# Optimization experiments

Hardware: AMD Instinct MI355X
Metric: run time of the kernel (lower is better)

Reference implementation:

```python
import jax, jax.numpy as jnp
import numpy as np

EPS = 1e-5
DEPTH = 6
HEADS = 8
DIM_HEAD = 64

def layer_norm(x, g, b):
    m = jnp.mean(x, axis=-1, keepdims=True)
    v = jnp.mean((x - m) ** 2, axis=-1, keepdims=True)
    return (x - m) * jax.lax.rsqrt(v + EPS) * g + b

def setup_inputs() -> dict:
    key = jax.random.key(0)
    ks = jax.random.split(key, 12)
    b, T, F, v, D = 4, 8, 16, 196, 768
    L, inner, ffh = DEPTH, HEADS * DIM_HEAD, 4 * D
    s = 0.02
    return {
        "x": jax.random.normal(ks[0], (b, T, F, v, D), jnp.float32),
        "latents": jax.random.normal(ks[1], (64, D), jnp.float32),
        "frame_emb": jax.random.normal(ks[2], (F, D), jnp.float32),
        "time_emb": jax.random.normal(ks[3], (T, 1, D), jnp.float32),
        "ln_m_g": jnp.ones((L, D), jnp.float32),
        "ln_m_b": jnp.zeros((L, D), jnp.float32),
        "ln_l_g": jnp.ones((L, D), jnp.float32),
        "ln_l_b": jnp.zeros((L, D), jnp.float32),
        "Wq": jax.random.normal(ks[4], (L, D, inner), jnp.float32) * s,
        "Wk": jax.random.normal(ks[5], (L, D, inner), jnp.float32) * s,
        "Wv": jax.random.normal(ks[6], (L, D, inner), jnp.float32) * s,
        "Wo": jax.random.normal(ks[7], (L, inner, D), jnp.float32) * s,
        "ff_ln_g": jnp.ones((L, D), jnp.float32),
        "ff_ln_b": jnp.zeros((L, D), jnp.float32),
        "W1": jax.random.normal(ks[8], (L, D, ffh), jnp.float32) * s,
        "W2": jax.random.normal(ks[9], (L, ffh, D), jnp.float32) * s,
        "out_ln_g": jnp.ones((D,), jnp.float32),
        "out_ln_b": jnp.zeros((D,), jnp.float32),
    }

def perceiver_attention(x, lat, g_m, b_m, g_l, b_l, Wq, Wk, Wv, Wo):
    # x: [b, Nx, D], lat: [b, Nz, D]
    b, Nz, D = lat.shape
    xm = layer_norm(x, g_m, b_m)
    ln = layer_norm(lat, g_l, b_l)
    q = (ln @ Wq).reshape(b, Nz, HEADS, DIM_HEAD).transpose(0, 2, 1, 3)  # b h q d
    kv = jnp.concatenate([xm, ln], axis=1)  # b (Nx+Nz) D
    Nf = kv.shape[1]
    k = (kv @ Wk).reshape(b, Nf, HEADS, DIM_HEAD).transpose(0, 2, 1, 3)
    v = (kv @ Wv).reshape(b, Nf, HEADS, DIM_HEAD).transpose(0, 2, 1, 3)
    q = q * (DIM_HEAD ** -0.5)
    sim = jnp.einsum('bhqd,bhfd->bhqf', q, k)
    alphas = jax.nn.softmax(sim, axis=-1)
    out = jnp.einsum('bhqf,bhfd->bhqd', alphas, v)
    out = out.transpose(0, 2, 1, 3).reshape(b, Nz, HEADS * DIM_HEAD)
    return out @ Wo

def reference(x, latents, frame_emb, time_emb, ln_m_g, ln_m_b, ln_l_g, ln_l_b,
              Wq, Wk, Wv, Wo, ff_ln_g, ff_ln_b, W1, W2, out_ln_g, out_ln_b):
    b, T, F, v, D = x.shape
    x = x + frame_emb[:F][None, None, :, None, :]           # frame embeddings
    x = x.reshape(b, T, F * v, D)
    x = x + time_emb[:T][None]                              # time pos embeddings (broadcast over n)
    x = x.reshape(b, T * F * v, D)
    lat = jnp.broadcast_to(latents[None], (b,) + latents.shape)
    for i in range(DEPTH):
        lat = lat + perceiver_attention(x, lat, ln_m_g[i], ln_m_b[i], ln_l_g[i], ln_l_b[i],
                                        Wq[i], Wk[i], Wv[i], Wo[i])
        h = layer_norm(lat, ff_ln_g[i], ff_ln_b[i])
        lat = lat + jax.nn.gelu(h @ W1[i], approximate=False) @ W2[i]
    return layer_norm(lat, out_ln_g, out_ln_b)
```

## Files before the change

### kernel.cpp

```cpp
#include <hip/hip_runtime.h>
#include <cstdint>
#include <cstddef>

typedef unsigned short u16;
typedef __attribute__((ext_vector_type(8))) short short8;
typedef __attribute__((ext_vector_type(4))) float f4;

#define LNEPS 1e-5f

__device__ __forceinline__ float b2f(u16 u){
  union { unsigned u; float f; } x; x.u = ((unsigned)u) << 16; return x.f;
}
__device__ __forceinline__ u16 f2b(float f){
  union { float f; unsigned u; } x; x.f = f;
  unsigned r = x.u + 0x7fffu + ((x.u >> 16) & 1u);
  return (u16)(r >> 16);
}
__device__ __forceinline__ float ldin(const void* p, long i, int f){
  return f ? ((const float*)p)[i] : b2f(((const u16*)p)[i]);
}

__global__ void detect_k(const u16* __restrict__ g1, int* __restrict__ flag) {
  int isf32 = 1, isbf = 1;
  for (int i = 0; i < 8; i++) {
    if (g1[2 * i] != 0 || g1[2 * i + 1] != 0x3F80) isf32 = 0;
    if (g1[i] != 0x3F80) isbf = 0;
  }
  *flag = (isf32 && !isbf) ? 1 : 0;
}

__global__ void cvt_k(const void* __restrict__ in, u16* __restrict__ out, long n,
                      const int* __restrict__ flag) {
  int f = *flag;
  for (long i = (long)blockIdx.x * 256 + threadIdx.x; i < n; i += (long)gridDim.x * 256)
    out[i] = f ? f2b(((const float*)in)[i]) : ((const u16*)in)[i];
}

__global__ __launch_bounds__(256) void transpose_in(const void* __restrict__ in,
                                                    u16* __restrict__ out,
                                                    int R, int C, long inZ, long outZ,
                                                    const int* __restrict__ flag) {
  __shared__ u16 tile[32][33];
  int f = *flag;
  long ib = (long)blockIdx.z * inZ;
  u16* op = out + (long)blockIdx.z * outZ;
  int c0 = blockIdx.x * 32, r0 = blockIdx.y * 32;
  int tx = threadIdx.x & 31, ty = threadIdx.x >> 5;
  #pragma unroll
  for (int k = 0; k < 4; k++) {
    int ry = ty + 8 * k;
    long idx = ib + (long)(r0 + ry) * C + c0 + tx;
    tile[ry][tx] = f ? f2b(((const float*)in)[idx]) : ((const u16*)in)[idx];
  }
  __syncthreads();
  #pragma unroll
  for (int k = 0; k < 4; k++) {
    int cy = ty + 8 * k;
    op[(long)(c0 + cy) * R + r0 + tx] = tile[tx][cy];
  }
}

__global__ __launch_bounds__(256) void transpose_b16(const u16* __restrict__ in,
                                                     u16* __restrict__ out,
                                                     int R, int C, long inZ, long outZ) {
  __shared__ u16 tile[32][33];
  const u16* ip = in + (long)blockIdx.z * inZ;
  u16* op = out + (long)blockIdx.z * outZ;
  int c0 = blockIdx.x * 32, r0 = blockIdx.y * 32;
  int tx = threadIdx.x & 31, ty = threadIdx.x >> 5;
  #pragma unroll
  for (int k = 0; k < 4; k++) {
    int ry = ty + 8 * k;
    tile[ry][tx] = ip[(long)(r0 + ry) * C + c0 + tx];
  }
  __syncthreads();
  #pragma unroll
  for (int k = 0; k < 4; k++) {
    int cy = ty + 8 * k;
    op[(long)(c0 + cy) * R + r0 + tx] = tile[tx][cy];
  }
}

__global__ __launch_bounds__(256) void compute_xn_k(const void* __restrict__ x,
                                                    const void* __restrict__ fe,
                                                    const void* __restrict__ te,
                                                    u16* __restrict__ xn,
                                                    const int* __restrict__ flag) {
  int f = *flag;
  long r = blockIdx.x;
  int rem = (int)(r % 25088);
  int tt = rem / 3136;
  int fi = (rem % 3136) / 196;
  int t = threadIdx.x;
  float vals[3]; float s = 0.f, s2 = 0.f;
  #pragma unroll
  for (int i = 0; i < 3; i++) {
    int c = t + 256 * i;
    float v = ldin(x, r * 768 + c, f) + ldin(fe, (long)fi * 768 + c, f)
            + ldin(te, (long)tt * 768 + c, f);
    vals[i] = v; s += v; s2 += v * v;
  }
  __shared__ float red[8];
  #pragma unroll
  for (int m = 32; m; m >>= 1) { s += __shfl_xor(s, m); s2 += __shfl_xor(s2, m); }
  int w = t >> 6;
  if ((t & 63) == 0) { red[w] = s; red[4 + w] = s2; }
  __syncthreads();
  float S = red[0] + red[1] + red[2] + red[3];
  float S2 = red[4] + red[5] + red[6] + red[7];
  float mean = S * (1.f / 768.f);
  float var = S2 * (1.f / 768.f) - mean * mean;
  float inv = rsqrtf(var + LNEPS);
  #pragma unroll
  for (int i = 0; i < 3; i++) {
    int c = t + 256 * i;
    xn[r * 768 + c] = f2b((vals[i] - mean) * inv);
  }
}

__global__ __launch_bounds__(256) void ln_rows_k(const float* __restrict__ src,
                                                 const u16* __restrict__ g,
                                                 const u16* __restrict__ bb,
                                                 void* __restrict__ dst,
                                                 const int* __restrict__ flag,
                                                 int outSel) {
  int of32 = outSel ? *flag : 0;
  long r = blockIdx.x;
  const float* xr = src + r * 768;
  int t = threadIdx.x;
  float vals[3]; float s = 0.f, s2 = 0.f;
  #pragma unroll
  for (int i = 0; i < 3; i++) {
    float v = xr[t + 256 * i]; vals[i] = v; s += v; s2 += v * v;
  }
  __shared__ float red[8];
  #pragma unroll
  for (int m = 32; m; m >>= 1) { s += __shfl_xor(s, m); s2 += __shfl_xor(s2, m); }
  int w = t >> 6;
  if ((t & 63) == 0) { red[w] = s; red[4 + w] = s2; }
  __syncthreads();
  float S = red[0] + red[1] + red[2] + red[3];
  float S2 = red[4] + red[5] + red[6] + red[7];
  float mean = S * (1.f / 768.f);
  float var = S2 * (1.f / 768.f) - mean * mean;
  float inv = rsqrtf(var + LNEPS);
  #pragma unroll
  for (int i = 0; i < 3; i++) {
    int c = t + 256 * i;
    float v = (vals[i] - mean) * inv * b2f(g[c]) + b2f(bb[c]);
    if (of32) ((float*)dst)[r * 768 + c] = v;
    else      ((u16*)dst)[r * 768 + c] = f2b(v);
  }
}

__global__ void init_lat_k(const void* __restrict__ latents, float* __restrict__ lat,
                           const int* __restrict__ flag) {
  int f = *flag;
  long i = (long)blockIdx.x * 256 + threadIdx.x;
  lat[i] = ldin(latents, i % 49152, f);
}

__global__ void zero_f32_k(float* __restrict__ p, long n) {
  for (long i = (long)blockIdx.x * 256 + threadIdx.x; i < n; i += (long)gridDim.x * 256)
    p[i] = 0.f;
}

__global__ void report_k(u16* out, float v) { out[0] = f2b(v); }

__global__ __launch_bounds__(256) void bias_proj_k(const u16* __restrict__ bm,
                                                   const u16* __restrict__ WkT,
                                                   const u16* __restrict__ WvT,
                                                   float* __restrict__ bk,
                                                   float* __restrict__ bv) {
  int t = blockIdx.x * 256 + threadIdx.x;
  int j = t & 511;
  const u16* row = ((t >> 9) ? WvT : WkT) + (long)j * 768;
  float s = 0.f;
  for (int d = 0; d < 768; d++) s += b2f(bm[d]) * b2f(row[d]);
  ((t >> 9) ? bv : bk)[j] = s;
}

__global__ __launch_bounds__(256) void prep_small_k(const u16* __restrict__ qkv,
                                                    const float* __restrict__ bk,
                                                    float* __restrict__ s_lat,
                                                    float* __restrict__ latmax,
                                                    float* __restrict__ cbias) {
  int t = threadIdx.x; int wv = t >> 6, lane = t & 63;
  int r = blockIdx.x * 4 + wv;
  int b = r >> 9, hq = r & 511, h = hq >> 6, qi = hq & 63;
  const u16* qrow = qkv + ((long)(b * 64 + qi)) * 1536 + h * 64;
  const u16* krow = qkv + ((long)(b * 64 + lane)) * 1536 + 512 + h * 64;
  float s = 0.f;
  for (int d = 0; d < 64; d++) s += b2f(qrow[d]) * b2f(krow[d]);
  s *= 0.125f;
  s_lat[(long)r * 64 + lane] = s;
  float cb = b2f(qrow[lane]) * bk[h * 64 + lane];
  float mx = s;
  #pragma unroll
  for (int m = 32; m; m >>= 1) { mx = fmaxf(mx, __shfl_xor(mx, m)); cb += __shfl_xor(cb, m); }
  if (lane == 0) { latmax[r] = mx; cbias[r] = 0.125f * cb; }
}

__global__ __launch_bounds__(256) void softmax_rows_k(u16* __restrict__ St,
                                                      const float* __restrict__ latmax,
                                                      const float* __restrict__ s_lat,
                                                      float* __restrict__ mrow,
                                                      float* __restrict__ sxrow,
                                                      float* __restrict__ linv) {
  const int NCH = 3136;
  long r = blockIdx.x;
  uint4* row4 = (uint4*)(St + r * 25088L);
  int t = threadIdx.x; int lane = t & 63, w = t >> 6;
  __shared__ float red[8];
  float mx = -3e38f;
  for (int c = t; c < NCH; c += 256) {
    uint4 u = row4[c];
    mx = fmaxf(mx, b2f((u16)(u.x & 0xffff))); mx = fmaxf(mx, b2f((u16)(u.x >> 16)));
    mx = fmaxf(mx, b2f((u16)(u.y & 0xffff))); mx = fmaxf(mx, b2f((u16)(u.y >> 16)));
    mx = fmaxf(mx, b2f((u16)(u.z & 0xffff))); mx = fmaxf(mx, b2f((u16)(u.z >> 16)));
    mx = fmaxf(mx, b2f((u16)(u.w & 0xffff))); mx = fmaxf(mx, b2f((u16)(u.w >> 16)));
  }
  #pragma unroll
  for (int m = 32; m; m >>= 1) mx = fmaxf(mx, __shfl_xor(mx, m));
  if (lane == 0) red[w] = mx;
  __syncthreads();
  float mv = fmaxf(fmaxf(red[0], red[1]), fmaxf(red[2], red[3]));
  mv = fmaxf(mv, latmax[r]);
  __syncthreads();
  if (w == 0) {
    float e = expf(s_lat[r * 64 + lane] - mv);
    #pragma unroll
    for (int m = 32; m; m >>= 1) e += __shfl_xor(e, m);
    if (lane == 0) red[4] = e;
  }
  float sum = 0.f;
  for (int c = t; c < NCH; c += 256) {
    uint4 u = row4[c];
    float e0 = expf(b2f((u16)(u.x & 0xffff)) - mv), e1 = expf(b2f((u16)(u.x >> 16)) - mv);
    float e2 = expf(b2f((u16)(u.y & 0xffff)) - mv), e3 = expf(b2f((u16)(u.y >> 16)) - mv);
    float e4 = expf(b2f((u16)(u.z & 0xffff)) - mv), e5 = expf(b2f((u16)(u.z >> 16)) - mv);
    float e6 = expf(b2f((u16)(u.w & 0xffff)) - mv), e7 = expf(b2f((u16)(u.w >> 16)) - mv);
    sum += ((e0 + e1) + (e2 + e3)) + ((e4 + e5) + (e6 + e7));
    u.x = (unsigned)f2b(e0) | ((unsigned)f2b(e1) << 16);
    u.y = (unsigned)f2b(e2) | ((unsigned)f2b(e3) << 16);
    u.z = (unsigned)f2b(e4) | ((unsigned)f2b(e5) << 16);
    u.w = (unsigned)f2b(e6) | ((unsigned)f2b(e7) << 16);
    row4[c] = u;
  }
  #pragma unroll
  for (int m = 32; m; m >>= 1) sum += __shfl_xor(sum, m);
  if (lane == 0) red[w] = sum;
  __syncthreads();
  if (t == 0) {
    float sx = red[0] + red[1] + red[2] + red[3];
    mrow[r] = mv; sxrow[r] = sx;
    linv[r] = 1.0f / (sx + red[4]);
  }
}

__global__ void ctxg_k(const float* __restrict__ CTX, const u16* __restrict__ gm,
                       u16* __restrict__ CTXg, long n) {
  for (long i = (long)blockIdx.x * 256 + threadIdx.x; i < n; i += (long)gridDim.x * 256) {
    int c = (int)(i % 768);
    CTXg[i] = f2b(CTX[i] * b2f(gm[c]));
  }
}

__global__ __launch_bounds__(256) void out_lat_k(const u16* __restrict__ qkv,
                                                 const float* __restrict__ s_lat,
                                                 const float* __restrict__ mrow,
                                                 float* __restrict__ out_lat) {
  int t = threadIdx.x; int wv = t >> 6, lane = t & 63;
  int r = blockIdx.x * 4 + wv;
  int b = r >> 9, hq = r & 511, h = hq >> 6;
  float mv = mrow[r];
  const u16* vbase = qkv + ((long)(b * 64)) * 1536 + 1024 + h * 64 + lane;
  float a = 0.f;
  for (int fl = 0; fl < 64; fl++)
    a += expf(s_lat[(long)r * 64 + fl] - mv) * b2f(vbase[(long)fl * 1536]);
  out_lat[(long)r * 64 + lane] = a;
}

struct GemmP {
  const u16* A; const u16* B; void* C;
  long lda, ldb, ldc;
  int M, N, K, kPerSplit, mtiles, numH;
  long aSB, aSH, bSB, bSH, cSB, cSH;
  float scale;
  const float* rowBias;
  const u16* colScaleB;
  const float* sxv; const float* colBiasF; const float* addMat; const float* rowScale;
};

__device__ __forceinline__ void glds16(const u16* g, u16* l) {
  __builtin_amdgcn_global_load_lds((const __attribute__((address_space(1))) void*)g,
                                   (__attribute__((address_space(3))) void*)l, 16, 0, 0);
}

template <int EPI>
__global__ __launch_bounds__(256, 2) void gemm_bt(GemmP p) {
  __shared__ u16 As[4096];
  __shared__ u16 Bs[4096];
  const int t = threadIdx.x;
  const int z = blockIdx.z;
  const int zb = z / p.numH, zh = z - zb * p.numH;
  const u16* A = p.A + (long)zb * p.aSB + (long)zh * p.aSH;
  const u16* B = p.B + (long)zb * p.bSB + (long)zh * p.bSH;
  const int mt = blockIdx.y % p.mtiles;
  const int split = blockIdx.y / p.mtiles;
  const int tm = mt * 128, tn = blockIdx.x * 128;
  const int K0 = split * p.kPerSplit;
  const int Kend = min(p.K, K0 + p.kPerSplit);

  const int c0 = t, c1 = t + 256;
  const int ko0 = c0 >> 7, mm0 = c0 & 127;
  const int ko1 = c1 >> 7, mm1 = c1 & 127;
  const int ra0 = min(tm + mm0, p.M - 1);
  const int ra1 = min(tm + mm1, p.M - 1);
  const int rb0 = min(tn + mm0, p.N - 1);
  const int rb1 = min(tn + mm1, p.N - 1);
  const u16* pa0 = A + (long)ra0 * p.lda + ko0 * 8;
  const u16* pa1 = A + (long)ra1 * p.lda + ko1 * 8;
  const u16* pb0 = B + (long)rb0 * p.ldb + ko0 * 8;
  const u16* pb1 = B + (long)rb1 * p.ldb + ko1 * 8;
  u16* la0 = As + c0 * 8; u16* la1 = As + c1 * 8;
  u16* lb0 = Bs + c0 * 8; u16* lb1 = Bs + c1 * 8;

  const int lane = t & 63, w = t >> 6;
  const int wm = w >> 1, wn = w & 1;
  const int lm = lane & 15, lg = lane >> 4;
  const u16* lA = As + (lg * 128 + wm * 64 + lm) * 8;
  const u16* lB = Bs + (lg * 128 + wn * 64 + lm) * 8;

  f4 acc[4][4];
  #pragma unroll
  for (int i = 0; i < 4; i++)
    #pragma unroll
    for (int j = 0; j < 4; j++) acc[i][j] = f4{0.f, 0.f, 0.f, 0.f};

  for (int kk = K0; kk < Kend; kk += 32) {
    __syncthreads();
    glds16(pa0 + kk, la0);
    glds16(pa1 + kk, la1);
    glds16(pb0 + kk, lb0);
    glds16(pb1 + kk, lb1);
    __syncthreads();
    short8 av[4], bvf[4];
    #pragma unroll
    for (int i = 0; i < 4; i++) av[i] = *(const short8*)(lA + i * 128);
    #pragma unroll
    for (int j = 0; j < 4; j++) bvf[j] = *(const short8*)(lB + j * 128);
    #pragma unroll
    for (int i = 0; i < 4; i++)
      #pragma unroll
      for (int j = 0; j < 4; j++)
        acc[i][j] = __builtin_amdgcn_mfma_f32_16x16x32_bf16(av[i], bvf[j], acc[i][j], 0, 0, 0);
  }

  u16* Cb = (u16*)p.C + (long)zb * p.cSB + (long)zh * p.cSH;
  float* Cf = (float*)p.C + (long)zb * p.cSB + (long)zh * p.cSH;
  #pragma unroll
  for (int i = 0; i < 4; i++) {
    #pragma unroll
    for (int j = 0; j < 4; j++) {
      int col = tn + wn * 64 + j * 16 + lm;
      int row0 = tm + wm * 64 + i * 16 + lg * 4;
      #pragma unroll
      for (int rr = 0; rr < 4; rr++) {
        int row = row0 + rr;
        if (row < p.M && col < p.N) {
          float v = acc[i][j][rr] * p.scale;
          if constexpr (EPI == 0) {
            Cb[(long)row * p.ldc + col] = f2b(v);
          } else if constexpr (EPI == 2) {
            atomicAdd(&Cf[(long)row * p.ldc + col], v);
          } else if constexpr (EPI == 3) {
            v += p.rowBias[(long)zb * p.M + row];
            Cb[(long)row * p.ldc + col] = f2b(v);
          } else if constexpr (EPI == 4) {
            float g = 0.5f * v * (1.0f + erff(v * 0.70710678118f));
            Cb[(long)row * p.ldc + col] = f2b(g);
          } else if constexpr (EPI == 5) {
            int hq = zh * 64 + row;
            long rb = (long)zb * 512 + hq;
            v = (v + p.sxv[rb] * p.colBiasF[zh * 64 + col] + p.addMat[rb * 64 + col]) * p.rowScale[rb];
            Cb[(long)row * p.ldc + col] = f2b(v);
          } else if constexpr (EPI == 6) {
            v *= b2f(p.colScaleB[col]);
            Cb[(long)row * p.ldc + col] = f2b(v);
          }
        }
      }
    }
  }
}

static inline void gemm_launch(int epi, dim3 g, const GemmP& p, hipStream_t s) {
  switch (epi) {
    case 0: gemm_bt<0><<<g, 256, 0, s>>>(p); break;
    case 2: gemm_bt<2><<<g, 256, 0, s>>>(p); break;
    case 3: gemm_bt<3><<<g, 256, 0, s>>>(p); break;
    case 4: gemm_bt<4><<<g, 256, 0, s>>>(p); break;
    case 5: gemm_bt<5><<<g, 256, 0, s>>>(p); break;
    case 6: gemm_bt<6><<<g, 256, 0, s>>>(p); break;
  }
}

extern "C" void kernel_launch(void* const* d_in, const int* in_sizes, int n_in,
                              void* d_out, int out_size, void* d_ws, size_t ws_size,
                              hipStream_t stream) {
  (void)in_sizes; (void)n_in; (void)out_size;
  const void* x      = d_in[0];
  const void* lats   = d_in[1];
  const void* frame  = d_in[2];
  const void* timee  = d_in[3];
  const void* ln_m_g = d_in[4];
  const void* ln_m_b = d_in[5];
  const void* ln_l_g = d_in[6];
  const void* ln_l_b = d_in[7];
  const void* Wq     = d_in[8];
  const void* Wk     = d_in[9];
  const void* Wv     = d_in[10];
  const void* Wo     = d_in[11];
  const void* ff_g   = d_in[12];
  const void* ff_b   = d_in[13];
  const void* W1     = d_in[14];
  const void* W2     = d_in[15];
  const void* og     = d_in[16];
  const void* ob     = d_in[17];

  char* ws = (char*)d_ws;
  size_t off = 0;
  auto alloc = [&](size_t bytes) -> char* {
    char* p = ws + off;
    off = (off + bytes + 255) & ~(size_t)255;
    return p;
  };
  int*   flag  = (int*)alloc(4);
  u16*   Xn    = (u16*)alloc(77070336ULL * 2);
  u16*   XnT   = (u16*)alloc(77070336ULL * 2);
  u16*   St    = (u16*)alloc(51380224ULL * 2);
  u16*   WT3   = (u16*)alloc(7077888ULL * 2);
  u16*   WoT   = (u16*)alloc(2359296ULL * 2);
  u16*   W1T   = (u16*)alloc(14155776ULL * 2);
  u16*   W2T   = (u16*)alloc(14155776ULL * 2);
  u16*   WkC   = (u16*)alloc(2359296ULL * 2);
  u16*   pMg   = (u16*)alloc(4608ULL * 2);
  u16*   pMb   = (u16*)alloc(4608ULL * 2);
  u16*   pLg   = (u16*)alloc(4608ULL * 2);
  u16*   pLb   = (u16*)alloc(4608ULL * 2);
  u16*   pFg   = (u16*)alloc(4608ULL * 2);
  u16*   pFb   = (u16*)alloc(4608ULL * 2);
  u16*   pOg   = (u16*)alloc(768ULL * 2);
  u16*   pOb   = (u16*)alloc(768ULL * 2);
  float* lat   = (float*)alloc(196608ULL * 4);
  u16*   lnb   = (u16*)alloc(196608ULL * 2);
  u16*   qkv   = (u16*)alloc(393216ULL * 2);
  u16*   QT    = (u16*)alloc(1572864ULL * 2);
  float* s_lat = (float*)alloc(131072ULL * 4);
  float* bk    = (float*)alloc(512 * 4);
  float* bvv   = (float*)alloc(512 * 4);
  float* cbias = (float*)alloc(2048 * 4);
  float* latmx = (float*)alloc(2048 * 4);
  float* mrow  = (float*)alloc(2048 * 4);
  float* sxrow = (float*)alloc(2048 * 4);
  float* linv  = (float*)alloc(2048 * 4);
  float* CTX   = (float*)alloc(1572864ULL * 4);
  u16*   CTXg  = (u16*)alloc(1572864ULL * 2);
  float* outl  = (float*)alloc(131072ULL * 4);
  u16*   ao    = (u16*)alloc(131072ULL * 2);
  u16*   hbuf  = (u16*)alloc(196608ULL * 2);
  u16*   t1g   = (u16*)alloc(786432ULL * 2);

  if (off > ws_size) {
    report_k<<<1, 1, 0, stream>>>((u16*)d_out, (float)ws_size);
    return;
  }

  detect_k<<<1, 1, 0, stream>>>((const u16*)ln_m_g, flag);
  cvt_k<<<18, 256, 0, stream>>>(ln_m_g, pMg, 4608, flag);
  cvt_k<<<18, 256, 0, stream>>>(ln_m_b, pMb, 4608, flag);
  cvt_k<<<18, 256, 0, stream>>>(ln_l_g, pLg, 4608, flag);
  cvt_k<<<18, 256, 0, stream>>>(ln_l_b, pLb, 4608, flag);
  cvt_k<<<18, 256, 0, stream>>>(ff_g, pFg, 4608, flag);
  cvt_k<<<18, 256, 0, stream>>>(ff_b, pFb, 4608, flag);
  cvt_k<<<3, 256, 0, stream>>>(og, pOg, 768, flag);
  cvt_k<<<3, 256, 0, stream>>>(ob, pOb, 768, flag);
  cvt_k<<<2048, 256, 0, stream>>>(Wk, WkC, 2359296, flag);

  transpose_in<<<dim3(16, 24, 6), 256, 0, stream>>>(Wq, WT3 + 0 * 393216, 768, 512, 393216, 1179648, flag);
  transpose_in<<<dim3(16, 24, 6), 256, 0, stream>>>(Wk, WT3 + 1 * 393216, 768, 512, 393216, 1179648, flag);
  transpose_in<<<dim3(16, 24, 6), 256, 0, stream>>>(Wv, WT3 + 2 * 393216, 768, 512, 393216, 1179648, flag);
  transpose_in<<<dim3(24, 16, 6), 256, 0, stream>>>(Wo, WoT, 512, 768, 393216, 393216, flag);
  transpose_in<<<dim3(96, 24, 6), 256, 0, stream>>>(W1, W1T, 768, 3072, 2359296, 2359296, flag);
  transpose_in<<<dim3(24, 96, 6), 256, 0, stream>>>(W2, W2T, 3072, 768, 2359296, 2359296, flag);
  compute_xn_k<<<100352, 256, 0, stream>>>(x, frame, timee, Xn, flag);
  transpose_b16<<<dim3(24, 784, 4), 256, 0, stream>>>(Xn, XnT, 25088, 768, 19267584, 19267584);
  init_lat_k<<<768, 256, 0, stream>>>(lats, lat, flag);

  for (int l = 0; l < 6; l++) {
    const u16* WkC_l = WkC + (long)l * 393216;
    const u16* WT3_l = WT3 + (long)l * 1179648;

    ln_rows_k<<<256, 256, 0, stream>>>(lat, pLg + l * 768, pLb + l * 768, lnb, flag, 0);

    {
      GemmP p{}; p.A = lnb; p.B = WT3_l; p.C = qkv;
      p.lda = 768; p.ldb = 768; p.ldc = 1536;
      p.M = 256; p.N = 1536; p.K = 768; p.kPerSplit = 768; p.mtiles = 2; p.numH = 1;
      p.scale = 1.f;
      gemm_launch(0, dim3(12, 2, 1), p, stream);
    }
    {
      GemmP p{}; p.A = qkv; p.B = WkC_l; p.C = QT;
      p.lda = 1536; p.ldb = 512; p.ldc = 768;
      p.M = 64; p.N = 768; p.K = 64; p.kPerSplit = 64; p.mtiles = 1; p.numH = 8;
      p.aSB = 98304; p.aSH = 64; p.bSB = 0; p.bSH = 64; p.cSB = 393216; p.cSH = 49152;
      p.scale = 0.125f; p.colScaleB = pMg + l * 768;
      gemm_launch(6, dim3(6, 1, 32), p, stream);
    }
    bias_proj_k<<<4, 256, 0, stream>>>(pMb + l * 768, WT3_l + 393216, WT3_l + 786432, bk, bvv);
    prep_small_k<<<512, 256, 0, stream>>>(qkv, bk, s_lat, latmx, cbias);
    zero_f32_k<<<1536, 256, 0, stream>>>(CTX, 1572864);

    {
      GemmP p{}; p.A = QT; p.B = Xn; p.C = St;
      p.lda = 768; p.ldb = 768; p.ldc = 25088;
      p.M = 512; p.N = 25088; p.K = 768; p.kPerSplit = 768; p.mtiles = 4; p.numH = 1;
      p.aSB = 393216; p.bSB = 19267584; p.cSB = 12845056;
      p.scale = 1.f; p.rowBias = cbias;
      gemm_launch(3, dim3(196, 4, 4), p, stream);
    }
    softmax_rows_k<<<2048, 256, 0, stream>>>(St, latmx, s_lat, mrow, sxrow, linv);

    {
      GemmP p{}; p.A = St; p.B = XnT; p.C = CTX;
      p.lda = 25088; p.ldb = 25088; p.ldc = 768;
      p.M = 512; p.N = 768; p.K = 25088; p.kPerSplit = 3136; p.mtiles = 4; p.numH = 1;
      p.aSB = 12845056; p.bSB = 19267584; p.cSB = 393216;
      p.scale = 1.f;
      gemm_launch(2, dim3(6, 32, 4), p, stream);
    }
    ctxg_k<<<1536, 256, 0, stream>>>(CTX, pMg + l * 768, CTXg, 1572864);
    out_lat_k<<<512, 256, 0, stream>>>(qkv, s_lat, mrow, outl);

    {
      GemmP p{}; p.A = CTXg; p.B = WT3_l + 2 * 393216; p.C = ao;
      p.lda = 768; p.ldb = 768; p.ldc = 512;
      p.M = 64; p.N = 64; p.K = 768; p.kPerSplit = 768; p.mtiles = 1; p.numH = 8;
      p.aSB = 393216; p.aSH = 49152; p.bSB = 0; p.bSH = 49152; p.cSB = 32768; p.cSH = 64;
      p.scale = 1.f; p.sxv = sxrow; p.colBiasF = bvv; p.addMat = outl; p.rowScale = linv;
      gemm_launch(5, dim3(1, 1, 32), p, stream);
    }
    {
      GemmP p{}; p.A = ao; p.B = WoT + (long)l * 393216; p.C = lat;
      p.lda = 512; p.ldb = 512; p.ldc = 768;
      p.M = 256; p.N = 768; p.K = 512; p.kPerSplit = 512; p.mtiles = 2; p.numH = 1;
      p.scale = 1.f;
      gemm_launch(2, dim3(6, 2, 1), p, stream);
    }
    ln_rows_k<<<256, 256, 0, stream>>>(lat, pFg + l * 768, pFb + l * 768, hbuf, flag, 0);
    {
      GemmP p{}; p.A = hbuf; p.B = W1T + (long)l * 2359296; p.C = t1g;
      p.lda = 768; p.ldb = 768; p.ldc = 3072;
      p.M = 256; p.N = 3072; p.K = 768; p.kPerSplit = 768; p.mtiles = 2; p.numH = 1;
      p.scale = 1.f;
      gemm_launch(4, dim3(24, 2, 1), p, stream);
    }
    {
      GemmP p{}; p.A = t1g; p.B = W2T + (long)l * 2359296; p.C = lat;
      p.lda = 3072; p.ldb = 3072; p.ldc = 768;
      p.M = 256; p.N = 768; p.K = 3072; p.kPerSplit = 768; p.mtiles = 2; p.numH = 1;
      p.scale = 1.f;
      gemm_launch(2, dim3(6, 8, 1), p, stream);
    }
  }
  ln_rows_k<<<256, 256, 0, stream>>>(lat, pOg, pOb, d_out, flag, 1);
}
```

Measured before the change: 5.202 ms.

## Double-buffer GEMM LDS tiles and remap blocks for XCD-aware scheduling

```diff
diff --git a/kernel.cpp b/kernel.cpp
--- a/kernel.cpp
+++ b/kernel.cpp
@@ -299,16 +299,28 @@
 
 template <int EPI>
 __global__ __launch_bounds__(256, 2) void gemm_bt(GemmP p) {
-  __shared__ u16 As[4096];
-  __shared__ u16 Bs[4096];
+  __shared__ u16 As[2][4096];
+  __shared__ u16 Bs[2][4096];
   const int t = threadIdx.x;
-  const int z = blockIdx.z;
+
+  const int gx = gridDim.x, gy = gridDim.y, gz = gridDim.z;
+  const int splits = gy / p.mtiles;
+  const long total = (long)gx * gy * gz;
+  const long fid = blockIdx.x + (long)gx * ((long)blockIdx.y + (long)gy * blockIdx.z);
+  const long qq = total >> 3, rr = total & 7;
+  const long xcd = fid & 7, idx = fid >> 3;
+  const long logical = (xcd < rr ? xcd * (qq + 1) : rr * (qq + 1) + (xcd - rr) * qq) + idx;
+  const int mt = (int)(logical % p.mtiles);
+  const long l1 = logical / p.mtiles;
+  const int bxn = (int)(l1 % gx);
+  const long l2 = l1 / gx;
+  const int split = (int)(l2 % splits);
+  const int z = (int)(l2 / splits);
+
   const int zb = z / p.numH, zh = z - zb * p.numH;
   const u16* A = p.A + (long)zb * p.aSB + (long)zh * p.aSH;
   const u16* B = p.B + (long)zb * p.bSB + (long)zh * p.bSH;
-  const int mt = blockIdx.y % p.mtiles;
-  const int split = blockIdx.y / p.mtiles;
-  const int tm = mt * 128, tn = blockIdx.x * 128;
+  const int tm = mt * 128, tn = bxn * 128;
   const int K0 = split * p.kPerSplit;
   const int Kend = min(p.K, K0 + p.kPerSplit);
 
@@ -323,14 +335,12 @@
   const u16* pa1 = A + (long)ra1 * p.lda + ko1 * 8;
   const u16* pb0 = B + (long)rb0 * p.ldb + ko0 * 8;
   const u16* pb1 = B + (long)rb1 * p.ldb + ko1 * 8;
-  u16* la0 = As + c0 * 8; u16* la1 = As + c1 * 8;
-  u16* lb0 = Bs + c0 * 8; u16* lb1 = Bs + c1 * 8;
 
   const int lane = t & 63, w = t >> 6;
   const int wm = w >> 1, wn = w & 1;
   const int lm = lane & 15, lg = lane >> 4;
-  const u16* lA = As + (lg * 128 + wm * 64 + lm) * 8;
-  const u16* lB = Bs + (lg * 128 + wn * 64 + lm) * 8;
+  const int lOffA = (lg * 128 + wm * 64 + lm) * 8;
+  const int lOffB = (lg * 128 + wn * 64 + lm) * 8;
 
   f4 acc[4][4];
   #pragma unroll
@@ -338,13 +348,23 @@
     #pragma unroll
     for (int j = 0; j < 4; j++) acc[i][j] = f4{0.f, 0.f, 0.f, 0.f};
 
+  glds16(pa0 + K0, &As[0][c0 * 8]);
+  glds16(pa1 + K0, &As[0][c1 * 8]);
+  glds16(pb0 + K0, &Bs[0][c0 * 8]);
+  glds16(pb1 + K0, &Bs[0][c1 * 8]);
+  __syncthreads();
+
+  int cur = 0;
   for (int kk = K0; kk < Kend; kk += 32) {
-    __syncthreads();
-    glds16(pa0 + kk, la0);
-    glds16(pa1 + kk, la1);
-    glds16(pb0 + kk, lb0);
-    glds16(pb1 + kk, lb1);
-    __syncthreads();
+    const int nxt = kk + 32;
+    if (nxt < Kend) {
+      glds16(pa0 + nxt, &As[cur ^ 1][c0 * 8]);
+      glds16(pa1 + nxt, &As[cur ^ 1][c1 * 8]);
+      glds16(pb0 + nxt, &Bs[cur ^ 1][c0 * 8]);
+      glds16(pb1 + nxt, &Bs[cur ^ 1][c1 * 8]);
+    }
+    const u16* lA = &As[cur][lOffA];
+    const u16* lB = &Bs[cur][lOffB];
     short8 av[4], bvf[4];
     #pragma unroll
     for (int i = 0; i < 4; i++) av[i] = *(const short8*)(lA + i * 128);
@@ -355,6 +375,8 @@
       #pragma unroll
       for (int j = 0; j < 4; j++)
         acc[i][j] = __builtin_amdgcn_mfma_f32_16x16x32_bf16(av[i], bvf[j], acc[i][j], 0, 0, 0);
+    __syncthreads();
+    cur ^= 1;
   }
 
   u16* Cb = (u16*)p.C + (long)zb * p.cSB + (long)zh * p.cSH;
@@ -366,10 +388,10 @@
       int col = tn + wn * 64 + j * 16 + lm;
       int row0 = tm + wm * 64 + i * 16 + lg * 4;
       #pragma unroll
-      for (int rr = 0; rr < 4; rr++) {
-        int row = row0 + rr;
+      for (int rr2 = 0; rr2 < 4; rr2++) {
+        int row = row0 + rr2;
         if (row < p.M && col < p.N) {
-          float v = acc[i][j][rr] * p.scale;
+          float v = acc[i][j][rr2] * p.scale;
           if constexpr (EPI == 0) {
             Cb[(long)row * p.ldc + col] = f2b(v);
           } else if constexpr (EPI == 2) {
```

Result: faster. 4.873 ms (-6.3%).
